# Optimization experiments

Hardware: AMD Instinct MI355X
Metric: run time of the kernel (lower is better)

## Reference

```python
import jax, jax.numpy as jnp
import numpy as np

EPS = 1e-5

def _layernorm_per_head(x, gamma, beta):
    # x: [b, h, L, d]; gamma, beta: [h, d] (distinct LayerNorm per head)
    mu = jnp.mean(x, axis=-1, keepdims=True)
    var = jnp.var(x, axis=-1, keepdims=True)
    xhat = (x - mu) * jax.lax.rsqrt(var + EPS)
    return xhat * gamma[None, :, None, :] + beta[None, :, None, :]

def setup_inputs() -> dict:
    key = jax.random.key(0)
    ks = jax.random.split(key, 10)
    b, nx, ny, nt = 2, 32, 32, 32
    cin, d, h = 128, 128, 8
    hd = h * d
    s_in = 1.0 / np.sqrt(cin)
    s_hd = 1.0 / np.sqrt(hd)
    return {
        "v": jax.random.normal(ks[0], (b, nx, ny, nt, cin), dtype=jnp.float32),
        "Wq_w": jax.random.normal(ks[1], (cin, hd), dtype=jnp.float32) * s_in,
        "Wq_b": jnp.zeros((hd,), dtype=jnp.float32),
        "Wk_w": jax.random.normal(ks[2], (cin, hd), dtype=jnp.float32) * s_in,
        "Wk_b": jnp.zeros((hd,), dtype=jnp.float32),
        "Wv_w": jax.random.normal(ks[3], (cin, hd), dtype=jnp.float32) * s_in,
        "Wv_b": jnp.zeros((hd,), dtype=jnp.float32),
        "Wo_w": jax.random.normal(ks[4], (hd, d), dtype=jnp.float32) * s_hd,
        "Wo_b": jnp.zeros((d,), dtype=jnp.float32),
        "lnk_g": jnp.ones((h, d), dtype=jnp.float32),
        "lnk_b": jnp.zeros((h, d), dtype=jnp.float32),
        "lnv_g": jnp.ones((h, d), dtype=jnp.float32),
        "lnv_b": jnp.zeros((h, d), dtype=jnp.float32),
    }

def reference(v, Wq_w, Wq_b, Wk_w, Wk_b, Wv_w, Wv_b, Wo_w, Wo_b,
              lnk_g, lnk_b, lnv_g, lnv_b):
    b, nx, ny, nt, cin = v.shape
    h, d = lnk_g.shape
    L = nx * ny * nt
    n = nx * ny  # NOTE: original divides by nx*ny only (not nt)
    x = v.reshape(b, L, cin)
    # projections -> [b, h, L, d]
    def proj(W, bias):
        y = x @ W + bias  # [b, L, h*d]
        return y.reshape(b, L, h, d).transpose(0, 2, 1, 3)
    Q = proj(Wq_w, Wq_b)
    K = proj(Wk_w, Wk_b)
    V = proj(Wv_w, Wv_b)
    K = _layernorm_per_head(K, lnk_g, lnk_b)
    V = _layernorm_per_head(V, lnv_g, lnv_b)
    # linear (Galerkin) attention: K^T V then Q (K^T V)
    attn_map = jnp.einsum('bhmd,bhmc->bhdc', K, V)      # [b, h, d, d]
    attn_out = jnp.einsum('bhld,bhdc->bhlc', Q, attn_map)  # [b, h, L, d]
    attn_out = attn_out.transpose(0, 2, 1, 3).reshape(b, L, h * d)
    out = (attn_out @ Wo_w + Wo_b) / n
    return out.reshape(b, nx, ny, nt, d)
```

## Files before the change

kernel.cpp:

```cpp
#include <hip/hip_runtime.h>
#include <stdint.h>

typedef unsigned short u16;
typedef unsigned int u32;
typedef __attribute__((ext_vector_type(8))) short s16x8;
typedef __attribute__((ext_vector_type(8))) __bf16 bf16x8;
typedef __attribute__((ext_vector_type(4))) float f32x4;
typedef __attribute__((ext_vector_type(4))) u16 u16x4;

#define L_TOT 32768
#define NCH 16

__device__ __forceinline__ u32 f2bf(float f){
  u32 u = __builtin_bit_cast(u32, f);
  return (u + 0x7FFFu + ((u >> 16) & 1u)) >> 16;
}
__device__ __forceinline__ u32 swz(u32 a){ return a ^ (((a >> 8) & 7u) << 4); }

__device__ __forceinline__ f32x4 mfma16(s16x8 a, s16x8 b, f32x4 c){
  return __builtin_amdgcn_mfma_f32_16x16x32_bf16(
      __builtin_bit_cast(bf16x8, a), __builtin_bit_cast(bf16x8, b), c, 0, 0, 0);
}

__device__ __forceinline__ void gload16(const void* g, void* l){
  __builtin_amdgcn_global_load_lds(
      (const __attribute__((address_space(1))) void*)g,
      (__attribute__((address_space(3))) void*)l, 16, 0, 0);
}

__device__ __forceinline__ u32 cvtpk(float lo, float hi){
  u32 r;
  asm("v_cvt_pk_bf16_f32 %0, %1, %2" : "=v"(r) : "v"(lo), "v"(hi));
  return r;
}

__device__ __forceinline__ float dpp_reduce16(float x){
  float y;
  asm("v_add_f32_dpp %0, %1, %1 row_ror:8 row_mask:0xf bank_mask:0xf"
      : "=&v"(y) : "v"(x));
  asm("v_add_f32_dpp %0, %1, %1 row_ror:4 row_mask:0xf bank_mask:0xf"
      : "=&v"(x) : "v"(y));
  asm("v_add_f32_dpp %0, %1, %1 quad_perm:[2,3,0,1] row_mask:0xf bank_mask:0xf"
      : "=&v"(y) : "v"(x));
  asm("v_add_f32_dpp %0, %1, %1 quad_perm:[1,0,3,2] row_mask:0xf bank_mask:0xf"
      : "=&v"(x) : "v"(y));
  return x;
}

__global__ void kprep(const float* __restrict__ v, const float* __restrict__ Wk,
                      const float* __restrict__ Wv, u16* __restrict__ X,
                      u16* __restrict__ WkT, u16* __restrict__ WvT){
  int tid = blockIdx.x * blockDim.x + threadIdx.x;
  int stride = gridDim.x * blockDim.x;
  for (int i = tid; i < 2097152; i += stride){
    float4 f = *((const float4*)v + i);
    u16x4 o; o.x = (u16)f2bf(f.x); o.y = (u16)f2bf(f.y); o.z = (u16)f2bf(f.z); o.w = (u16)f2bf(f.w);
    *((u16x4*)X + i) = o;
  }
  for (int i = tid; i < 131072; i += stride){
    int n = i >> 7, c = i & 127;
    WkT[i] = (u16)f2bf(Wk[c * 1024 + n]);
    WvT[i] = (u16)f2bf(Wv[c * 1024 + n]);
  }
}

__global__ __launch_bounds__(512, 2) void kattn(
    const u16* __restrict__ X, const u16* __restrict__ WkT, const u16* __restrict__ WvT,
    const float* __restrict__ bk, const float* __restrict__ bv,
    const float* __restrict__ gk, const float* __restrict__ bbk,
    const float* __restrict__ gv, const float* __restrict__ bbv,
    float* __restrict__ AM)
{
  extern __shared__ char smem[];
  char* sWk = smem;
  char* sWv = smem + 32768;
  char* sKT = smem + 65536;
  char* sVT = smem + 98304;

  const int tid = threadIdx.x;
  const int wid = tid >> 6, lane = tid & 63, g = lane >> 4, l15 = lane & 15;
  const int bh = blockIdx.x >> 4, grp = blockIdx.x & 15;
  const int b = bh >> 3, h = bh & 7;
  const bool isK = (wid < 4);
  const int w4 = wid & 3;

  {
    const char* gwk = (const char*)(WkT + h * 16384);
    const char* gwv = (const char*)(WvT + h * 16384);
    #pragma unroll
    for (int call = 0; call < 4; ++call){
      u32 o = (u32)(call * 8192 + wid * 1024 + lane * 16);
      gload16(gwk + swz(o), sWk + (call * 8192 + wid * 1024));
      gload16(gwv + swz(o), sWv + (call * 8192 + wid * 1024));
    }
  }
  const float* bias = isK ? bk : bv;
  const float* gam  = isK ? gk : gv;
  const float* beta = isK ? bbk : bbv;
  float br[8], gr[8], betar[8];
  #pragma unroll
  for (int nt = 0; nt < 8; ++nt){
    int idx = h * 128 + nt * 16 + l15;
    br[nt] = bias[idx]; gr[nt] = gam[idx]; betar[nt] = beta[idx];
  }
  asm volatile("s_waitcnt vmcnt(0)" ::: "memory");
  __builtin_amdgcn_s_barrier();

  f32x4 am[4][2];
  #pragma unroll
  for (int mt = 0; mt < 4; ++mt)
    #pragma unroll
    for (int nt = 0; nt < 2; ++nt) am[mt][nt] = f32x4{0.f, 0.f, 0.f, 0.f};

  const u16* Xb = X + (size_t)b * (L_TOT * 128);
  const char* sW = isK ? sWk : sWv;
  char* sT = isK ? sKT : sVT;

  auto pref = [&](s16x8 (&dst)[2][4], int chunk){
    int row0 = (grp * NCH + chunk) * 128;
    #pragma unroll
    for (int mt = 0; mt < 2; ++mt)
      #pragma unroll
      for (int ks = 0; ks < 4; ++ks){
        int r = row0 + w4 * 32 + mt * 16 + l15;
        dst[mt][ks] = *(const s16x8*)(Xb + (size_t)r * 128 + ks * 32 + g * 8);
      }
  };

  auto body = [&](const s16x8 (&af)[2][4]){
    f32x4 acc[2][8];
    #pragma unroll
    for (int mt = 0; mt < 2; ++mt)
      #pragma unroll
      for (int nt = 0; nt < 8; ++nt) acc[mt][nt] = f32x4{0.f, 0.f, 0.f, 0.f};
    #pragma unroll
    for (int ks = 0; ks < 4; ++ks){
      #pragma unroll
      for (int nt = 0; nt < 8; ++nt){
        u32 a = (u32)((nt * 16 + l15) * 256 + ks * 64 + g * 16);
        s16x8 bfr = *(const s16x8*)(sW + swz(a));
        acc[0][nt] = mfma16(af[0][ks], bfr, acc[0][nt]);
        acc[1][nt] = mfma16(af[1][ks], bfr, acc[1][nt]);
      }
    }
    #pragma unroll
    for (int mt = 0; mt < 2; ++mt){
      #pragma unroll
      for (int j = 0; j < 4; ++j){
        float s = 0.f, q = 0.f;
        float vv[8];
        #pragma unroll
        for (int nt = 0; nt < 8; ++nt){
          float t = acc[mt][nt][j] + br[nt];
          vv[nt] = t; s += t; q += t * t;
        }
        s = dpp_reduce16(s);
        q = dpp_reduce16(q);
        float mean = s * 0.0078125f;
        float var  = q * 0.0078125f - mean * mean;
        float rstd = rsqrtf(var + 1e-5f);
        #pragma unroll
        for (int nt = 0; nt < 8; ++nt)
          acc[mt][nt][j] = (vv[nt] - mean) * rstd * gr[nt] + betar[nt];
      }
      #pragma unroll
      for (int nt = 0; nt < 8; ++nt){
        int dk = nt * 16 + l15;
        int lc = w4 * 32 + mt * 16 + g * 4;
        u32 base = (u32)(dk * 256 + lc * 2);
        uint2 w; w.x = cvtpk(acc[mt][nt][0], acc[mt][nt][1]);
        w.y = cvtpk(acc[mt][nt][2], acc[mt][nt][3]);
        *(uint2*)(sT + swz(base)) = w;
      }
    }
    asm volatile("s_waitcnt lgkmcnt(0)" ::: "memory");
    __builtin_amdgcn_s_barrier();
    asm volatile("" ::: "memory");
    #pragma unroll
    for (int ks2 = 0; ks2 < 4; ++ks2){
      s16x8 a2[4], b2[2];
      #pragma unroll
      for (int mt2 = 0; mt2 < 4; ++mt2){
        int dk = (wid >> 2) * 64 + mt2 * 16 + l15;
        a2[mt2] = *(const s16x8*)(sKT + swz((u32)(dk * 256 + ks2 * 64 + g * 16)));
      }
      #pragma unroll
      for (int nt2 = 0; nt2 < 2; ++nt2){
        int dv = w4 * 32 + nt2 * 16 + l15;
        b2[nt2] = *(const s16x8*)(sVT + swz((u32)(dv * 256 + ks2 * 64 + g * 16)));
      }
      #pragma unroll
      for (int mt2 = 0; mt2 < 4; ++mt2)
        #pragma unroll
        for (int nt2 = 0; nt2 < 2; ++nt2)
          am[mt2][nt2] = mfma16(a2[mt2], b2[nt2], am[mt2][nt2]);
    }
    __builtin_amdgcn_s_barrier();
    asm volatile("" ::: "memory");
  };

  s16x8 af[2][4], afn[2][4];
  pref(af, 0);
  for (int it2 = 0; it2 < NCH; it2 += 2){
    pref(afn, it2 + 1);
    body(af);
    pref(af, (it2 + 2 < NCH) ? it2 + 2 : it2);
    body(afn);
  }

  float* AMbh = AM + (size_t)bh * 16384;
  #pragma unroll
  for (int mt2 = 0; mt2 < 4; ++mt2)
    #pragma unroll
    for (int nt2 = 0; nt2 < 2; ++nt2)
      #pragma unroll
      for (int j = 0; j < 4; ++j){
        int dk = (wid >> 2) * 64 + mt2 * 16 + g * 4 + j;
        int dv = w4 * 32 + nt2 * 16 + l15;
        atomicAdd(AMbh + dk * 128 + dv, am[mt2][nt2][j]);
      }
}

__global__ __launch_bounds__(256) void kfold(
    const float* __restrict__ AM, const float* __restrict__ Wo,
    const float* __restrict__ Wq, const float* __restrict__ Wq_b,
    const float* __restrict__ Wo_b,
    float* __restrict__ W4, float* __restrict__ c4)
{
  extern __shared__ float fsm[];
  float* sA = fsm;
  float* sS = fsm + 128 * 129;
  int blk = blockIdx.x;
  int bh = blk >> 2, eq = blk & 3;
  int b = bh >> 3, hs = bh & 7;
  int tid = threadIdx.x;

  for (int idx = tid; idx < 16384; idx += 256){
    int r = idx >> 7, c = idx & 127;
    sA[r * 129 + c] = AM[(size_t)bh * 16384 + idx];
  }
  for (int idx = tid; idx < 4096; idx += 256){
    int r = idx >> 5, c = idx & 31;
    sS[r * 33 + c] = Wo[(size_t)hs * 16384 + r * 128 + eq * 32 + c];
  }
  __syncthreads();

  int r0 = (tid >> 4) * 8, e0 = (tid & 15) * 2;
  float t8[8][2] = {};
  for (int c = 0; c < 128; ++c){
    float wv0 = sS[c * 33 + e0], wv1 = sS[c * 33 + e0 + 1];
    #pragma unroll
    for (int i = 0; i < 8; ++i){
      float a = sA[(r0 + i) * 129 + c];
      t8[i][0] += a * wv0; t8[i][1] += a * wv1;
    }
  }
  __syncthreads();
  #pragma unroll
  for (int i = 0; i < 8; ++i){
    sS[(r0 + i) * 33 + e0]     = t8[i][0];
    sS[(r0 + i) * 33 + e0 + 1] = t8[i][1];
  }
  for (int idx = tid; idx < 16384; idx += 256){
    int r = idx >> 7, c = idx & 127;
    sA[r * 129 + c] = Wq[(size_t)r * 1024 + hs * 128 + c];
  }
  __syncthreads();

  float a8[8][2] = {};
  for (int d = 0; d < 128; ++d){
    float t0 = sS[d * 33 + e0], t1 = sS[d * 33 + e0 + 1];
    #pragma unroll
    for (int i = 0; i < 8; ++i){
      float w = sA[(r0 + i) * 129 + d];
      a8[i][0] += w * t0; a8[i][1] += w * t1;
    }
  }
  const float inv_n = 0.0009765625f;
  #pragma unroll
  for (int i = 0; i < 8; ++i){
    atomicAdd(W4 + (size_t)b * 16384 + (r0 + i) * 128 + eq * 32 + e0,     a8[i][0] * inv_n);
    atomicAdd(W4 + (size_t)b * 16384 + (r0 + i) * 128 + eq * 32 + e0 + 1, a8[i][1] * inv_n);
  }
  if (tid < 32){
    float s = 0.f;
    for (int d = 0; d < 128; ++d) s += Wq_b[hs * 128 + d] * sS[d * 33 + tid];
    if (hs == 0) s += Wo_b[eq * 32 + tid];
    atomicAdd(c4 + b * 128 + eq * 32 + tid, s * inv_n);
  }
}

__global__ void kfold3(const float* __restrict__ W4, u16* __restrict__ W4T){
  int i = blockIdx.x * 256 + threadIdx.x;
  if (i >= 32768) return;
  int b = i >> 14, r = i & 16383, e = r >> 7, c = r & 127;
  W4T[i] = (u16)f2bf(W4[(size_t)b * 16384 + c * 128 + e]);
}

__global__ __launch_bounds__(256, 2) void kout(
    const u16* __restrict__ X, const u16* __restrict__ W4T,
    const float* __restrict__ c4, float* __restrict__ out)
{
  extern __shared__ char smem[];
  char* sX = smem; char* sW = smem + 32768;
  int tid = threadIdx.x, wid = tid >> 6, lane = tid & 63, g = lane >> 4, l15 = lane & 15;
  int blk = blockIdx.x; int b = blk >> 8, ch = blk & 255;
  const char* gx = (const char*)(X + ((size_t)b * L_TOT + ch * 128) * 128);
  const char* gw = (const char*)(W4T + (size_t)b * 16384);
  #pragma unroll
  for (int call = 0; call < 8; ++call){
    u32 o = (u32)(call * 4096 + wid * 1024 + lane * 16);
    gload16(gx + swz(o), sX + (call * 4096 + wid * 1024));
    gload16(gw + swz(o), sW + (call * 4096 + wid * 1024));
  }
  asm volatile("s_waitcnt vmcnt(0)" ::: "memory");
  __syncthreads();

  f32x4 acc[2][8];
  #pragma unroll
  for (int mt = 0; mt < 2; ++mt)
    #pragma unroll
    for (int nt = 0; nt < 8; ++nt) acc[mt][nt] = f32x4{0.f, 0.f, 0.f, 0.f};

  #pragma unroll
  for (int ks = 0; ks < 4; ++ks){
    s16x8 a0, a1;
    {
      int r = wid * 32 + l15;
      a0 = *(const s16x8*)(sX + swz((u32)(r * 256 + ks * 64 + g * 16)));
      a1 = *(const s16x8*)(sX + swz((u32)((r + 16) * 256 + ks * 64 + g * 16)));
    }
    #pragma unroll
    for (int nt = 0; nt < 8; ++nt){
      int e = nt * 16 + l15;
      s16x8 bfr = *(const s16x8*)(sW + swz((u32)(e * 256 + ks * 64 + g * 16)));
      acc[0][nt] = mfma16(a0, bfr, acc[0][nt]);
      acc[1][nt] = mfma16(a1, bfr, acc[1][nt]);
    }
  }
  float* ob = out + ((size_t)b * L_TOT + ch * 128) * 128;
  #pragma unroll
  for (int nt = 0; nt < 8; ++nt){
    float c4v = c4[b * 128 + nt * 16 + l15];
    #pragma unroll
    for (int mt = 0; mt < 2; ++mt)
      #pragma unroll
      for (int j = 0; j < 4; ++j){
        int r = wid * 32 + mt * 16 + g * 4 + j;
        ob[r * 128 + nt * 16 + l15] = acc[mt][nt][j] + c4v;
      }
  }
}

extern "C" void kernel_launch(void* const* d_in, const int* in_sizes, int n_in,
                              void* d_out, int out_size, void* d_ws, size_t ws_size,
                              hipStream_t stream){
  const float* v    = (const float*)d_in[0];
  const float* Wq_w = (const float*)d_in[1];
  const float* Wq_b = (const float*)d_in[2];
  const float* Wk_w = (const float*)d_in[3];
  const float* Wk_b = (const float*)d_in[4];
  const float* Wv_w = (const float*)d_in[5];
  const float* Wv_b = (const float*)d_in[6];
  const float* Wo_w = (const float*)d_in[7];
  const float* Wo_b = (const float*)d_in[8];
  const float* lnk_g = (const float*)d_in[9];
  const float* lnk_b = (const float*)d_in[10];
  const float* lnv_g = (const float*)d_in[11];
  const float* lnv_b = (const float*)d_in[12];

  char* ws = (char*)d_ws;
  u16*   X   = (u16*)  (ws);
  u16*   WkT = (u16*)  (ws + 16777216);
  u16*   WvT = (u16*)  (ws + 17039360);
  float* AM  = (float*)(ws + 17301504);
  float* W4  = (float*)(ws + 18350080);
  float* c4  = (float*)(ws + 18481152);
  u16*   W4T = (u16*)  (ws + 19530752);

  hipMemsetAsync(ws + 17301504, 0, 1180672, stream);

  hipLaunchKernelGGL(kprep, dim3(2048), dim3(256), 0, stream, v, Wk_w, Wv_w, X, WkT, WvT);

  (void)hipFuncSetAttribute((const void*)kattn,
                            hipFuncAttributeMaxDynamicSharedMemorySize, 131072);
  hipLaunchKernelGGL(kattn, dim3(256), dim3(512), 131072, stream,
                     X, WkT, WvT, Wk_b, Wv_b, lnk_g, lnk_b, lnv_g, lnv_b, AM);

  (void)hipFuncSetAttribute((const void*)kfold,
                            hipFuncAttributeMaxDynamicSharedMemorySize, 83968);
  hipLaunchKernelGGL(kfold, dim3(64), dim3(256), 83968, stream,
                     AM, Wo_w, Wq_w, Wq_b, Wo_b, W4, c4);
  hipLaunchKernelGGL(kfold3, dim3(128), dim3(256), 0, stream, W4, W4T);

  hipLaunchKernelGGL(kout, dim3(512), dim3(256), 65536, stream, X, W4T, c4, (float*)d_out);
}
```

Measured before the change: 148.0 us.

## Reformulate K^T V via per-row LayerNorm scales and a weighted input Gram matrix

Replaces the fused projection+LayerNorm+K^T V kernel with an algebraic decomposition. A stats kernel computes only the per-row rstd of K and V. A second kernel forms a weighted Gram matrix of the input, X^T diag(rk*rv) X, plus row-sum terms from a pre-transposed, fragment-ordered copy of X. The attention map is then rebuilt in fp32 from the weights, biases and LayerNorm parameters, and kout loads the folded weight directly in fragment order. The aim is to avoid materialising normalised K/V tiles in LDS and the per-chunk barriers, at the cost of extra kernels, a large partial-sum buffer with a reduction pass, a transposed copy of X, and possible precision changes from the var = E[x^2]-mu^2 algebra.

Measured after the change: 275.5 us. +86.1%, slower.

```diff
diff --git a/kernel.cpp b/kernel.cpp
--- a/kernel.cpp
+++ b/kernel.cpp
@@ -6,16 +6,13 @@
 typedef __attribute__((ext_vector_type(8))) short s16x8;
 typedef __attribute__((ext_vector_type(8))) __bf16 bf16x8;
 typedef __attribute__((ext_vector_type(4))) float f32x4;
+typedef __attribute__((ext_vector_type(4))) u32 u32x4;
 typedef __attribute__((ext_vector_type(4))) u16 u16x4;
-
-#define L_TOT 32768
-#define NCH 16
 
 __device__ __forceinline__ u32 f2bf(float f){
   u32 u = __builtin_bit_cast(u32, f);
   return (u + 0x7FFFu + ((u >> 16) & 1u)) >> 16;
 }
-__device__ __forceinline__ u32 swz(u32 a){ return a ^ (((a >> 8) & 7u) << 4); }
 
 __device__ __forceinline__ f32x4 mfma16(s16x8 a, s16x8 b, f32x4 c){
   return __builtin_amdgcn_mfma_f32_16x16x32_bf16(
@@ -47,185 +44,365 @@
   return x;
 }
 
-__global__ void kprep(const float* __restrict__ v, const float* __restrict__ Wk,
-                      const float* __restrict__ Wv, u16* __restrict__ X,
-                      u16* __restrict__ WkT, u16* __restrict__ WvT){
-  int tid = blockIdx.x * blockDim.x + threadIdx.x;
-  int stride = gridDim.x * blockDim.x;
-  for (int i = tid; i < 2097152; i += stride){
-    float4 f = *((const float4*)v + i);
-    u16x4 o; o.x = (u16)f2bf(f.x); o.y = (u16)f2bf(f.y); o.z = (u16)f2bf(f.z); o.w = (u16)f2bf(f.w);
-    *((u16x4*)X + i) = o;
-  }
-  for (int i = tid; i < 131072; i += stride){
-    int n = i >> 7, c = i & 127;
-    WkT[i] = (u16)f2bf(Wk[c * 1024 + n]);
-    WvT[i] = (u16)f2bf(Wv[c * 1024 + n]);
-  }
-}
-
-__global__ __launch_bounds__(512, 2) void kattn(
-    const u16* __restrict__ X, const u16* __restrict__ WkT, const u16* __restrict__ WvT,
+__device__ __forceinline__ void unpack8(s16x8 v, float* f){
+  u32x4 u = __builtin_bit_cast(u32x4, v);
+  #pragma unroll
+  for (int i = 0; i < 4; ++i){
+    f[2*i]   = __builtin_bit_cast(float, u[i] << 16);
+    f[2*i+1] = __builtin_bit_cast(float, u[i] & 0xffff0000u);
+  }
+}
+
+__global__ __launch_bounds__(256) void kprep(
+    const float* __restrict__ v, const float* __restrict__ Wk, const float* __restrict__ Wv,
+    const float* __restrict__ Wkb, const float* __restrict__ Wvb,
+    u16* __restrict__ X, u16* __restrict__ XTF, u16* __restrict__ WF,
+    float* __restrict__ w1u, float* __restrict__ scn)
+{
+  const int tid = threadIdx.x;
+  if (blockIdx.x < 512){
+    __shared__ u16 sx[128 * 132];
+    const int blk = blockIdx.x, b = blk >> 8, lch = blk & 255;
+    const float* vb = v + ((size_t)b * 32768 + lch * 128) * 128;
+    u16* xb = X + ((size_t)b * 32768 + lch * 128) * 128;
+    #pragma unroll
+    for (int i = 0; i < 16; ++i){
+      int flat = i * 1024 + tid * 4;
+      int r = flat >> 7, c = flat & 127;
+      float4 f = *(const float4*)(vb + flat);
+      u16x4 o; o.x = (u16)f2bf(f.x); o.y = (u16)f2bf(f.y); o.z = (u16)f2bf(f.z); o.w = (u16)f2bf(f.w);
+      *(u16x4*)(xb + flat) = o;
+      *(u16x4*)(&sx[r * 132 + c]) = o;
+    }
+    __syncthreads();
+    #pragma unroll
+    for (int it = 0; it < 8; ++it){
+      int t = it * 256 + tid;
+      int l15 = t & 15, gg = (t >> 4) & 3, lc = (t >> 6) & 3, ct = t >> 8;
+      u16 tmp[8];
+      #pragma unroll
+      for (int e = 0; e < 8; ++e)
+        tmp[e] = sx[(lc * 32 + gg * 8 + e) * 132 + ct * 16 + l15];
+      u32 w0 = (u32)tmp[0] | ((u32)tmp[1] << 16);
+      u32 w1_ = (u32)tmp[2] | ((u32)tmp[3] << 16);
+      u32 w2 = (u32)tmp[4] | ((u32)tmp[5] << 16);
+      u32 w3 = (u32)tmp[6] | ((u32)tmp[7] << 16);
+      u32x4 uu = {w0, w1_, w2, w3};
+      size_t off = ((((size_t)b * 8 + ct) * 1024 + (lch * 4 + lc)) * 4 + gg) * 128 + (size_t)l15 * 8;
+      *reinterpret_cast<u32x4*>(XTF + off) = uu;
+    }
+  } else {
+    const int hp = blockIdx.x - 512, h = hp & 7, proj = hp >> 3;
+    const float* W = proj ? Wv : Wk;
+    const float* pb = (proj ? Wvb : Wkb) + h * 128;
+    for (int i = tid; i < 16384; i += 256){
+      int e = i & 7, ln = (i >> 3) & 63, ks = (i >> 9) & 3, nt = i >> 11;
+      int c = ks * 32 + (ln >> 4) * 8 + e;
+      int n = nt * 16 + (ln & 15);
+      WF[proj * 131072 + h * 16384 + i] = (u16)f2bf(W[(size_t)c * 1024 + h * 128 + n]);
+    }
+    if (tid < 128){
+      float s = 0.f;
+      const float* p = W + (size_t)tid * 1024 + h * 128;
+      for (int n = 0; n < 128; ++n) s += p[n];
+      w1u[hp * 128 + tid] = s * 0.0078125f;
+    }
+    if (tid == 0){
+      float mb = 0.f;
+      for (int n = 0; n < 128; ++n) mb += pb[n];
+      scn[hp] = mb * 0.0078125f;
+    }
+  }
+}
+
+__global__ __launch_bounds__(512, 2) void kstat(
+    const u16* __restrict__ X, const u16* __restrict__ WF,
     const float* __restrict__ bk, const float* __restrict__ bv,
+    float* __restrict__ cF, u16* __restrict__ cab)
+{
+  extern __shared__ char sW[];
+  const int tid = threadIdx.x, wid = tid >> 6, lane = tid & 63, g = lane >> 4, l15 = lane & 15;
+  const int bh = blockIdx.x >> 4, grp = blockIdx.x & 15;
+  const int b = bh >> 3, h = bh & 7;
+  {
+    const char* wk = (const char*)(WF + h * 16384);
+    const char* wv = (const char*)(WF + 131072 + h * 16384);
+    #pragma unroll
+    for (int i = 0; i < 4; ++i){
+      u32 o = i * 8192 + tid * 16;
+      gload16(wk + o, sW + o);
+      gload16(wv + o, sW + 32768 + o);
+    }
+  }
+  float br[2][8];
+  #pragma unroll
+  for (int nt = 0; nt < 8; ++nt){
+    br[0][nt] = bk[h * 128 + nt * 16 + l15];
+    br[1][nt] = bv[h * 128 + nt * 16 + l15];
+  }
+  asm volatile("s_waitcnt vmcnt(0)" ::: "memory");
+  __builtin_amdgcn_s_barrier();
+
+  const u16* Xb = X + (size_t)b * 32768 * 128;
+  float* cFb = cF + (size_t)bh * 32768;
+  u16* cabb = cab + (size_t)bh * 3 * 32768;
+
+  #pragma unroll 1
+  for (int it = 0; it < 4; ++it){
+    const int rb = grp * 2048 + it * 512 + wid * 64;
+    s16x8 af[4][4];
+    #pragma unroll
+    for (int mt = 0; mt < 4; ++mt)
+      #pragma unroll
+      for (int ks = 0; ks < 4; ++ks)
+        af[mt][ks] = *(const s16x8*)(Xb + (size_t)(rb + mt * 16 + l15) * 128 + ks * 32 + g * 8);
+    float rst[2][4][4];
+    #pragma unroll
+    for (int pj = 0; pj < 2; ++pj){
+      f32x4 acc[4][8];
+      #pragma unroll
+      for (int mt = 0; mt < 4; ++mt)
+        #pragma unroll
+        for (int nt = 0; nt < 8; ++nt) acc[mt][nt] = f32x4{0.f, 0.f, 0.f, 0.f};
+      #pragma unroll
+      for (int ks = 0; ks < 4; ++ks)
+        #pragma unroll
+        for (int nt = 0; nt < 8; ++nt){
+          s16x8 wf = *(const s16x8*)(sW + pj * 32768 + (nt * 4 + ks) * 1024 + lane * 16);
+          #pragma unroll
+          for (int mt = 0; mt < 4; ++mt)
+            acc[mt][nt] = mfma16(af[mt][ks], wf, acc[mt][nt]);
+        }
+      #pragma unroll
+      for (int mt = 0; mt < 4; ++mt){
+        f32x4 s4 = {0.f,0.f,0.f,0.f}, q4 = {0.f,0.f,0.f,0.f};
+        #pragma unroll
+        for (int nt = 0; nt < 8; ++nt){
+          f32x4 t = acc[mt][nt] + br[pj][nt];
+          s4 += t; q4 += t * t;
+        }
+        #pragma unroll
+        for (int j = 0; j < 4; ++j){
+          float ss = dpp_reduce16(s4[j]);
+          float qq = dpp_reduce16(q4[j]);
+          float mu = ss * 0.0078125f;
+          float var = qq * 0.0078125f - mu * mu;
+          rst[pj][mt][j] = rsqrtf(var + 1e-5f);
+        }
+      }
+    }
+    #pragma unroll
+    for (int mt = 0; mt < 4; ++mt)
+      #pragma unroll
+      for (int j = 0; j < 4; ++j){
+        if (l15 == g * 4 + j){
+          int row = rb + mt * 16 + l15;
+          float a = rst[0][mt][j], bb = rst[1][mt][j], c = a * bb;
+          cFb[row] = c;
+          cabb[row] = (u16)f2bf(c);
+          cabb[32768 + row] = (u16)f2bf(a);
+          cabb[65536 + row] = (u16)f2bf(bb);
+        }
+      }
+  }
+}
+
+__global__ __launch_bounds__(512, 4) void kS2(
+    const u16* __restrict__ XTF, const float* __restrict__ cF, const u16* __restrict__ cab,
+    float* __restrict__ Spart)
+{
+  const int tid = threadIdx.x, wid = tid >> 6, lane = tid & 63, g = lane >> 4, l15 = lane & 15;
+  const int bh = blockIdx.x >> 4, grp = blockIdx.x & 15;
+  const int b = bh >> 3;
+  const int mtp = wid & 3, nth = wid >> 2;
+  const u16* xtb = XTF + (size_t)b * 4194304;
+  const float* cFb = cF + (size_t)bh * 32768;
+  const u16* cab3 = cab + (size_t)bh * 3 * 32768 + (size_t)(l15 < 3 ? l15 : 0) * 32768;
+
+  f32x4 accC[2][4], accB[2], accS = {0.f,0.f,0.f,0.f}, accS8 = {0.f,0.f,0.f,0.f};
+  #pragma unroll
+  for (int m2 = 0; m2 < 2; ++m2){
+    accB[m2] = f32x4{0.f,0.f,0.f,0.f};
+    #pragma unroll
+    for (int q = 0; q < 4; ++q) accC[m2][q] = f32x4{0.f,0.f,0.f,0.f};
+  }
+  s16x8 bone;
+  { u32 o = (l15 == 0) ? 0x3F803F80u : 0u; u32x4 t = {o, o, o, o};
+    bone = __builtin_bit_cast(s16x8, t); }
+
+  #pragma unroll 1
+  for (int kst = 0; kst < 64; ++kst){
+    const int lcg = grp * 64 + kst;
+    const int l0 = lcg * 32;
+    const size_t base = (size_t)(lcg * 4 + g) * 128 + (size_t)l15 * 8;
+    float cs[8];
+    { const float* cp = cFb + l0 + g * 8;
+      float4 c0 = *(const float4*)cp, c1 = *(const float4*)(cp + 4);
+      cs[0]=c0.x; cs[1]=c0.y; cs[2]=c0.z; cs[3]=c0.w;
+      cs[4]=c1.x; cs[5]=c1.y; cs[6]=c1.z; cs[7]=c1.w; }
+    s16x8 aS[2];
+    #pragma unroll
+    for (int m2 = 0; m2 < 2; ++m2){
+      s16x8 a0 = *(const s16x8*)(xtb + (size_t)(2 * mtp + m2) * 524288 + base);
+      float fa[8]; unpack8(a0, fa);
+      u32x4 pv = { cvtpk(fa[0]*cs[0], fa[1]*cs[1]), cvtpk(fa[2]*cs[2], fa[3]*cs[3]),
+                   cvtpk(fa[4]*cs[4], fa[5]*cs[5]), cvtpk(fa[6]*cs[6], fa[7]*cs[7]) };
+      aS[m2] = __builtin_bit_cast(s16x8, pv);
+    }
+    s16x8 astr = *(const s16x8*)(cab3 + l0 + g * 8);
+    if (l15 >= 3){ u32x4 z = {0,0,0,0}; astr = __builtin_bit_cast(s16x8, z); }
+    #pragma unroll
+    for (int q = 0; q < 4; ++q){
+      s16x8 bf = *(const s16x8*)(xtb + (size_t)(4 * nth + q) * 524288 + base);
+      accC[0][q] = mfma16(aS[0], bf, accC[0][q]);
+      accC[1][q] = mfma16(aS[1], bf, accC[1][q]);
+      if (q == mtp) accS = mfma16(astr, bf, accS);
+    }
+    if (nth == 0){
+      accB[0] = mfma16(aS[0], bone, accB[0]);
+      accB[1] = mfma16(aS[1], bone, accB[1]);
+      if (wid == 0) accS8 = mfma16(astr, bone, accS8);
+    }
+  }
+  float* Sp = Spart + ((size_t)bh * 16 + grp) * 19008;
+  #pragma unroll
+  for (int m2 = 0; m2 < 2; ++m2)
+    #pragma unroll
+    for (int q = 0; q < 4; ++q)
+      #pragma unroll
+      for (int j = 0; j < 4; ++j)
+        Sp[((2*mtp + m2)*16 + g*4 + j) * 144 + (4*nth + q)*16 + l15] = accC[m2][q][j];
+  if (g == 0){
+    #pragma unroll
+    for (int j = 0; j < 3; ++j)
+      Sp[(128 + j) * 144 + wid * 16 + l15] = accS[j];
+  }
+  if (nth == 0 && l15 == 0){
+    #pragma unroll
+    for (int m2 = 0; m2 < 2; ++m2)
+      #pragma unroll
+      for (int j = 0; j < 4; ++j)
+        Sp[((2*mtp + m2)*16 + g*4 + j) * 144 + 128] = accB[m2][j];
+  }
+  if (wid == 0 && g == 0 && l15 == 0){
+    #pragma unroll
+    for (int j = 0; j < 3; ++j)
+      Sp[(128 + j) * 144 + 128] = accS8[j];
+  }
+}
+
+__global__ __launch_bounds__(256) void kred(const float* __restrict__ Spart, float* __restrict__ S){
+  int bh = blockIdx.x, r = blockIdx.y, c = threadIdx.x;
+  if (c >= 144) return;
+  float s = 0.f;
+  const float* p = Spart + (size_t)bh * 16 * 19008 + r * 144 + c;
+  #pragma unroll
+  for (int gq = 0; gq < 16; ++gq) s += p[(size_t)gq * 19008];
+  S[(size_t)bh * 19008 + r * 144 + c] = s;
+}
+
+__global__ __launch_bounds__(256) void kfoldA(
+    const float* __restrict__ S, const float* __restrict__ Wk, const float* __restrict__ Wv,
+    const float* __restrict__ Wkb, const float* __restrict__ Wvb,
+    const float* __restrict__ w1u, const float* __restrict__ scn,
     const float* __restrict__ gk, const float* __restrict__ bbk,
     const float* __restrict__ gv, const float* __restrict__ bbv,
     float* __restrict__ AM)
 {
-  extern __shared__ char smem[];
-  char* sWk = smem;
-  char* sWv = smem + 32768;
-  char* sKT = smem + 65536;
-  char* sVT = smem + 98304;
-
+  extern __shared__ float fsm[];
+  float* sA = fsm;
+  float* sS = fsm + 16512;
+  float* svt = fsm + 20736;
+  float* svb = fsm + 20768;
+  float* skt = fsm + 20800;
+  float* skb = fsm + 20928;
+  const int blk = blockIdx.x, bh = blk >> 2, es = blk & 3;
+  const int h = bh & 7;
   const int tid = threadIdx.x;
-  const int wid = tid >> 6, lane = tid & 63, g = lane >> 4, l15 = lane & 15;
-  const int bh = blockIdx.x >> 4, grp = blockIdx.x & 15;
-  const int b = bh >> 3, h = bh & 7;
-  const bool isK = (wid < 4);
-  const int w4 = wid & 3;
-
-  {
-    const char* gwk = (const char*)(WkT + h * 16384);
-    const char* gwv = (const char*)(WvT + h * 16384);
-    #pragma unroll
-    for (int call = 0; call < 4; ++call){
-      u32 o = (u32)(call * 8192 + wid * 1024 + lane * 16);
-      gload16(gwk + swz(o), sWk + (call * 8192 + wid * 1024));
-      gload16(gwv + swz(o), sWv + (call * 8192 + wid * 1024));
-    }
-  }
-  const float* bias = isK ? bk : bv;
-  const float* gam  = isK ? gk : gv;
-  const float* beta = isK ? bbk : bbv;
-  float br[8], gr[8], betar[8];
-  #pragma unroll
-  for (int nt = 0; nt < 8; ++nt){
-    int idx = h * 128 + nt * 16 + l15;
-    br[nt] = bias[idx]; gr[nt] = gam[idx]; betar[nt] = beta[idx];
-  }
-  asm volatile("s_waitcnt vmcnt(0)" ::: "memory");
-  __builtin_amdgcn_s_barrier();
-
-  f32x4 am[4][2];
-  #pragma unroll
-  for (int mt = 0; mt < 4; ++mt)
-    #pragma unroll
-    for (int nt = 0; nt < 2; ++nt) am[mt][nt] = f32x4{0.f, 0.f, 0.f, 0.f};
-
-  const u16* Xb = X + (size_t)b * (L_TOT * 128);
-  const char* sW = isK ? sWk : sWv;
-  char* sT = isK ? sKT : sVT;
-
-  auto pref = [&](s16x8 (&dst)[2][4], int chunk){
-    int row0 = (grp * NCH + chunk) * 128;
-    #pragma unroll
-    for (int mt = 0; mt < 2; ++mt)
-      #pragma unroll
-      for (int ks = 0; ks < 4; ++ks){
-        int r = row0 + w4 * 32 + mt * 16 + l15;
-        dst[mt][ks] = *(const s16x8*)(Xb + (size_t)r * 128 + ks * 32 + g * 8);
-      }
-  };
-
-  auto body = [&](const s16x8 (&af)[2][4]){
-    f32x4 acc[2][8];
-    #pragma unroll
-    for (int mt = 0; mt < 2; ++mt)
-      #pragma unroll
-      for (int nt = 0; nt < 8; ++nt) acc[mt][nt] = f32x4{0.f, 0.f, 0.f, 0.f};
-    #pragma unroll
-    for (int ks = 0; ks < 4; ++ks){
-      #pragma unroll
-      for (int nt = 0; nt < 8; ++nt){
-        u32 a = (u32)((nt * 16 + l15) * 256 + ks * 64 + g * 16);
-        s16x8 bfr = *(const s16x8*)(sW + swz(a));
-        acc[0][nt] = mfma16(af[0][ks], bfr, acc[0][nt]);
-        acc[1][nt] = mfma16(af[1][ks], bfr, acc[1][nt]);
-      }
-    }
-    #pragma unroll
-    for (int mt = 0; mt < 2; ++mt){
-      #pragma unroll
-      for (int j = 0; j < 4; ++j){
-        float s = 0.f, q = 0.f;
-        float vv[8];
-        #pragma unroll
-        for (int nt = 0; nt < 8; ++nt){
-          float t = acc[mt][nt][j] + br[nt];
-          vv[nt] = t; s += t; q += t * t;
-        }
-        s = dpp_reduce16(s);
-        q = dpp_reduce16(q);
-        float mean = s * 0.0078125f;
-        float var  = q * 0.0078125f - mean * mean;
-        float rstd = rsqrtf(var + 1e-5f);
-        #pragma unroll
-        for (int nt = 0; nt < 8; ++nt)
-          acc[mt][nt][j] = (vv[nt] - mean) * rstd * gr[nt] + betar[nt];
-      }
-      #pragma unroll
-      for (int nt = 0; nt < 8; ++nt){
-        int dk = nt * 16 + l15;
-        int lc = w4 * 32 + mt * 16 + g * 4;
-        u32 base = (u32)(dk * 256 + lc * 2);
-        uint2 w; w.x = cvtpk(acc[mt][nt][0], acc[mt][nt][1]);
-        w.y = cvtpk(acc[mt][nt][2], acc[mt][nt][3]);
-        *(uint2*)(sT + swz(base)) = w;
-      }
-    }
-    asm volatile("s_waitcnt lgkmcnt(0)" ::: "memory");
-    __builtin_amdgcn_s_barrier();
-    asm volatile("" ::: "memory");
-    #pragma unroll
-    for (int ks2 = 0; ks2 < 4; ++ks2){
-      s16x8 a2[4], b2[2];
-      #pragma unroll
-      for (int mt2 = 0; mt2 < 4; ++mt2){
-        int dk = (wid >> 2) * 64 + mt2 * 16 + l15;
-        a2[mt2] = *(const s16x8*)(sKT + swz((u32)(dk * 256 + ks2 * 64 + g * 16)));
-      }
-      #pragma unroll
-      for (int nt2 = 0; nt2 < 2; ++nt2){
-        int dv = w4 * 32 + nt2 * 16 + l15;
-        b2[nt2] = *(const s16x8*)(sVT + swz((u32)(dv * 256 + ks2 * 64 + g * 16)));
-      }
-      #pragma unroll
-      for (int mt2 = 0; mt2 < 4; ++mt2)
-        #pragma unroll
-        for (int nt2 = 0; nt2 < 2; ++nt2)
-          am[mt2][nt2] = mfma16(a2[mt2], b2[nt2], am[mt2][nt2]);
-    }
-    __builtin_amdgcn_s_barrier();
-    asm volatile("" ::: "memory");
-  };
-
-  s16x8 af[2][4], afn[2][4];
-  pref(af, 0);
-  for (int it2 = 0; it2 < NCH; it2 += 2){
-    pref(afn, it2 + 1);
-    body(af);
-    pref(af, (it2 + 2 < NCH) ? it2 + 2 : it2);
-    body(afn);
-  }
-
-  float* AMbh = AM + (size_t)bh * 16384;
-  #pragma unroll
-  for (int mt2 = 0; mt2 < 4; ++mt2)
-    #pragma unroll
-    for (int nt2 = 0; nt2 < 2; ++nt2)
-      #pragma unroll
-      for (int j = 0; j < 4; ++j){
-        int dk = (wid >> 2) * 64 + mt2 * 16 + g * 4 + j;
-        int dv = w4 * 32 + nt2 * 16 + l15;
-        atomicAdd(AMbh + dk * 128 + dv, am[mt2][nt2][j]);
-      }
-}
-
-__global__ __launch_bounds__(256) void kfold(
+  const float* Sg = S + (size_t)bh * 19008;
+  const float mbk = scn[h], mbv = scn[8 + h];
+
+  for (int idx = tid; idx < 16384; idx += 256){
+    int r = idx >> 7, c = idx & 127;
+    sA[r * 129 + c] = Sg[r * 144 + c];
+  }
+  for (int idx = tid; idx < 4096; idx += 256){
+    int c = idx >> 5, j = idx & 31;
+    sS[c * 33 + j] = Wv[(size_t)c * 1024 + h * 128 + es * 32 + j] - w1u[(8 + h) * 128 + c];
+  }
+  __syncthreads();
+  if (tid < 32){
+    float t = 0.f, tb = 0.f;
+    for (int c = 0; c < 128; ++c){
+      float wv = sS[c * 33 + tid];
+      t  += Sg[128 * 144 + c] * wv;
+      tb += Sg[130 * 144 + c] * wv;
+    }
+    svt[tid] = t;
+    svb[tid] = tb + Sg[130 * 144 + 128] * (Wvb[h * 128 + es * 32 + tid] - mbv);
+  }
+  const int r0 = (tid >> 4) * 8, e0 = (tid & 15) * 2;
+  float t8[8][2] = {};
+  for (int c = 0; c < 128; ++c){
+    float w0 = sS[c * 33 + e0], w1_ = sS[c * 33 + e0 + 1];
+    #pragma unroll
+    for (int i = 0; i < 8; ++i){
+      float a = sA[(r0 + i) * 129 + c];
+      t8[i][0] += a * w0; t8[i][1] += a * w1_;
+    }
+  }
+  __syncthreads();
+  #pragma unroll
+  for (int i = 0; i < 8; ++i){
+    sS[(r0 + i) * 33 + e0] = t8[i][0];
+    sS[(r0 + i) * 33 + e0 + 1] = t8[i][1];
+  }
+  for (int idx = tid; idx < 16384; idx += 256){
+    int c = idx >> 7, n = idx & 127;
+    sA[c * 129 + n] = Wk[(size_t)c * 1024 + h * 128 + n] - w1u[h * 128 + c];
+  }
+  __syncthreads();
+  if (tid < 128){
+    float t = 0.f, ta = 0.f;
+    for (int c = 0; c < 128; ++c){
+      float wk = sA[c * 129 + tid];
+      t  += Sg[128 * 144 + c] * wk;
+      ta += Sg[129 * 144 + c] * wk;
+    }
+    skt[tid] = t;
+    skb[tid] = ta + Sg[129 * 144 + 128] * (Wkb[h * 128 + tid] - mbk);
+  }
+  float g8[8][2] = {};
+  for (int c = 0; c < 128; ++c){
+    float t0 = sS[c * 33 + e0], t1 = sS[c * 33 + e0 + 1];
+    #pragma unroll
+    for (int i = 0; i < 8; ++i){
+      float wk = sA[c * 129 + (r0 + i)];
+      g8[i][0] += wk * t0; g8[i][1] += wk * t1;
+    }
+  }
+  __syncthreads();
+  const float s0 = Sg[128 * 144 + 128];
+  #pragma unroll
+  for (int i = 0; i < 8; ++i){
+    int n = r0 + i;
+    float btk = Wkb[h * 128 + n] - mbk;
+    #pragma unroll
+    for (int jj = 0; jj < 2; ++jj){
+      int j = e0 + jj, dv = es * 32 + j;
+      float btv = Wvb[h * 128 + dv] - mbv;
+      float G = g8[i][jj] + skt[n] * btv + btk * svt[j] + s0 * btk * btv;
+      float am = gk[h*128+n] * (gv[h*128+dv] * G + skb[n] * bbv[h*128+dv])
+               + bbk[h*128+n] * (gv[h*128+dv] * svb[j] + 32768.f * bbv[h*128+dv]);
+      AM[(size_t)bh * 16384 + n * 128 + dv] = am;
+    }
+  }
+}
+
+__global__ __launch_bounds__(256) void kfoldB(
     const float* __restrict__ AM, const float* __restrict__ Wo,
     const float* __restrict__ Wq, const float* __restrict__ Wq_b,
-    const float* __restrict__ Wo_b,
-    float* __restrict__ W4, float* __restrict__ c4)
+    const float* __restrict__ Wo_b, float* __restrict__ W4F, float* __restrict__ c4)
 {
   extern __shared__ float fsm[];
   float* sA = fsm;
@@ -278,10 +455,14 @@
   }
   const float inv_n = 0.0009765625f;
   #pragma unroll
-  for (int i = 0; i < 8; ++i){
-    atomicAdd(W4 + (size_t)b * 16384 + (r0 + i) * 128 + eq * 32 + e0,     a8[i][0] * inv_n);
-    atomicAdd(W4 + (size_t)b * 16384 + (r0 + i) * 128 + eq * 32 + e0 + 1, a8[i][1] * inv_n);
-  }
+  for (int i = 0; i < 8; ++i)
+    #pragma unroll
+    for (int j = 0; j < 2; ++j){
+      int cc = r0 + i, nn = eq * 32 + e0 + j;
+      int o = ((nn >> 4) * 4 + (cc >> 5)) * 512 + ((cc >> 3) & 3) * 128
+            + (nn & 15) * 8 + (cc & 7);
+      atomicAdd(W4F + (size_t)b * 16384 + o, a8[i][j] * inv_n);
+    }
   if (tid < 32){
     float s = 0.f;
     for (int d = 0; d < 128; ++d) s += Wq_b[hs * 128 + d] * sS[d * 33 + tid];
@@ -290,30 +471,30 @@
   }
 }
 
-__global__ void kfold3(const float* __restrict__ W4, u16* __restrict__ W4T){
-  int i = blockIdx.x * 256 + threadIdx.x;
-  if (i >= 32768) return;
-  int b = i >> 14, r = i & 16383, e = r >> 7, c = r & 127;
-  W4T[i] = (u16)f2bf(W4[(size_t)b * 16384 + c * 128 + e]);
-}
-
-__global__ __launch_bounds__(256, 2) void kout(
-    const u16* __restrict__ X, const u16* __restrict__ W4T,
+__global__ __launch_bounds__(256, 4) void kout(
+    const u16* __restrict__ X, const float* __restrict__ W4F,
     const float* __restrict__ c4, float* __restrict__ out)
 {
-  extern __shared__ char smem[];
-  char* sX = smem; char* sW = smem + 32768;
-  int tid = threadIdx.x, wid = tid >> 6, lane = tid & 63, g = lane >> 4, l15 = lane & 15;
-  int blk = blockIdx.x; int b = blk >> 8, ch = blk & 255;
-  const char* gx = (const char*)(X + ((size_t)b * L_TOT + ch * 128) * 128);
-  const char* gw = (const char*)(W4T + (size_t)b * 16384);
-  #pragma unroll
-  for (int call = 0; call < 8; ++call){
-    u32 o = (u32)(call * 4096 + wid * 1024 + lane * 16);
-    gload16(gx + swz(o), sX + (call * 4096 + wid * 1024));
-    gload16(gw + swz(o), sW + (call * 4096 + wid * 1024));
-  }
-  asm volatile("s_waitcnt vmcnt(0)" ::: "memory");
+  __shared__ char sW[32768];
+  const int tid = threadIdx.x, wid = tid >> 6, lane = tid & 63, g = lane >> 4, l15 = lane & 15;
+  const int blk = blockIdx.x, b = blk >> 8, ch = blk & 255;
+  {
+    const float* w4b = W4F + (size_t)b * 16384;
+    #pragma unroll
+    for (int it2 = 0; it2 < 16; ++it2){
+      int idx = it2 * 1024 + tid * 4;
+      float4 f = *(const float4*)(w4b + idx);
+      uint2 w; w.x = cvtpk(f.x, f.y); w.y = cvtpk(f.z, f.w);
+      *(uint2*)(sW + idx * 2) = w;
+    }
+  }
+  const char* xr = (const char*)(X + ((size_t)b * 32768 + ch * 128 + wid * 32 + l15) * 128) + g * 16;
+  s16x8 af[2][4];
+  #pragma unroll
+  for (int mt = 0; mt < 2; ++mt)
+    #pragma unroll
+    for (int ks = 0; ks < 4; ++ks)
+      af[mt][ks] = *(const s16x8*)(xr + mt * 4096 + ks * 64);
   __syncthreads();
 
   f32x4 acc[2][8];
@@ -322,33 +503,24 @@
     #pragma unroll
     for (int nt = 0; nt < 8; ++nt) acc[mt][nt] = f32x4{0.f, 0.f, 0.f, 0.f};
 
-  #pragma unroll
-  for (int ks = 0; ks < 4; ++ks){
-    s16x8 a0, a1;
-    {
-      int r = wid * 32 + l15;
-      a0 = *(const s16x8*)(sX + swz((u32)(r * 256 + ks * 64 + g * 16)));
-      a1 = *(const s16x8*)(sX + swz((u32)((r + 16) * 256 + ks * 64 + g * 16)));
-    }
+  const u32 wread = (u32)(lane * 16);
+  #pragma unroll
+  for (int ks = 0; ks < 4; ++ks)
     #pragma unroll
     for (int nt = 0; nt < 8; ++nt){
-      int e = nt * 16 + l15;
-      s16x8 bfr = *(const s16x8*)(sW + swz((u32)(e * 256 + ks * 64 + g * 16)));
-      acc[0][nt] = mfma16(a0, bfr, acc[0][nt]);
-      acc[1][nt] = mfma16(a1, bfr, acc[1][nt]);
-    }
-  }
-  float* ob = out + ((size_t)b * L_TOT + ch * 128) * 128;
+      s16x8 wf = *(const s16x8*)(sW + wread + (nt * 4 + ks) * 1024);
+      acc[0][nt] = mfma16(af[0][ks], wf, acc[0][nt]);
+      acc[1][nt] = mfma16(af[1][ks], wf, acc[1][nt]);
+    }
+  float* ob = out + ((size_t)b * 32768 + ch * 128 + wid * 32) * 128;
   #pragma unroll
   for (int nt = 0; nt < 8; ++nt){
     float c4v = c4[b * 128 + nt * 16 + l15];
     #pragma unroll
     for (int mt = 0; mt < 2; ++mt)
       #pragma unroll
-      for (int j = 0; j < 4; ++j){
-        int r = wid * 32 + mt * 16 + g * 4 + j;
-        ob[r * 128 + nt * 16 + l15] = acc[mt][nt][j] + c4v;
-      }
+      for (int j = 0; j < 4; ++j)
+        ob[(mt * 16 + g * 4 + j) * 128 + nt * 16 + l15] = acc[mt][nt][j] + c4v;
   }
 }
 
@@ -370,28 +542,43 @@
   const float* lnv_b = (const float*)d_in[12];
 
   char* ws = (char*)d_ws;
-  u16*   X   = (u16*)  (ws);
-  u16*   WkT = (u16*)  (ws + 16777216);
-  u16*   WvT = (u16*)  (ws + 17039360);
-  float* AM  = (float*)(ws + 17301504);
-  float* W4  = (float*)(ws + 18350080);
-  float* c4  = (float*)(ws + 18481152);
-  u16*   W4T = (u16*)  (ws + 19530752);
-
-  hipMemsetAsync(ws + 17301504, 0, 1180672, stream);
-
-  hipLaunchKernelGGL(kprep, dim3(2048), dim3(256), 0, stream, v, Wk_w, Wv_w, X, WkT, WvT);
-
-  (void)hipFuncSetAttribute((const void*)kattn,
-                            hipFuncAttributeMaxDynamicSharedMemorySize, 131072);
-  hipLaunchKernelGGL(kattn, dim3(256), dim3(512), 131072, stream,
-                     X, WkT, WvT, Wk_b, Wv_b, lnk_g, lnk_b, lnv_g, lnv_b, AM);
-
-  (void)hipFuncSetAttribute((const void*)kfold,
-                            hipFuncAttributeMaxDynamicSharedMemorySize, 83968);
-  hipLaunchKernelGGL(kfold, dim3(64), dim3(256), 83968, stream,
-                     AM, Wo_w, Wq_w, Wq_b, Wo_b, W4, c4);
-  hipLaunchKernelGGL(kfold3, dim3(128), dim3(256), 0, stream, W4, W4T);
-
-  hipLaunchKernelGGL(kout, dim3(512), dim3(256), 65536, stream, X, W4T, c4, (float*)d_out);
-}
+  u16*   X     = (u16*)  (ws);
+  u16*   XTF   = (u16*)  (ws + 16777216);
+  u16*   WF    = (u16*)  (ws + 33554432);
+  float* cF    = (float*)(ws + 34078720);
+  u16*   cab   = (u16*)  (ws + 36175872);
+  float* w1u   = (float*)(ws + 39321600);
+  float* scn   = (float*)(ws + 39329792);
+  float* Spart = (float*)(ws + 39329920);
+  float* S     = (float*)(ws + 58794112);
+  float* AM    = (float*)(ws + 60010624);
+  float* W4F   = (float*)(ws + 61059200);
+  float* c4    = (float*)(ws + 61190272);
+
+  hipMemsetAsync(ws + 61059200, 0, 132096, stream);
+
+  hipLaunchKernelGGL(kprep, dim3(528), dim3(256), 0, stream,
+                     v, Wk_w, Wv_w, Wk_b, Wv_b, X, XTF, WF, w1u, scn);
+
+  (void)hipFuncSetAttribute((const void*)kstat,
+                            hipFuncAttributeMaxDynamicSharedMemorySize, 65536);
+  hipLaunchKernelGGL(kstat, dim3(256), dim3(512), 65536, stream,
+                     X, WF, Wk_b, Wv_b, cF, cab);
+
+  hipLaunchKernelGGL(kS2, dim3(256), dim3(512), 0, stream, XTF, cF, cab, Spart);
+
+  hipLaunchKernelGGL(kred, dim3(16, 132), dim3(256), 0, stream, Spart, S);
+
+  (void)hipFuncSetAttribute((const void*)kfoldA,
+                            hipFuncAttributeMaxDynamicSharedMemorySize, 84224);
+  hipLaunchKernelGGL(kfoldA, dim3(64), dim3(256), 84224, stream,
+                     S, Wk_w, Wv_w, Wk_b, Wv_b, w1u, scn,
+                     lnk_g, lnk_b, lnv_g, lnv_b, AM);
+
+  (void)hipFuncSetAttribute((const void*)kfoldB,
+                            hipFuncAttributeMaxDynamicSharedMemorySize, 82944);
+  hipLaunchKernelGGL(kfoldB, dim3(64), dim3(256), 82944, stream,
+                     AM, Wo_w, Wq_w, Wq_b, Wo_b, W4F, c4);
+
+  hipLaunchKernelGGL(kout, dim3(512), dim3(256), 0, stream, X, W4F, c4, (float*)d_out);
+}
```
